# Optimization experiments

Measured on AMD Instinct MI355X. Metric: run time of the kernel, lower is better.

Reference implementation:

```python
import jax, jax.numpy as jnp
import numpy as np

N_NODES = 20000
N_EDGES = 320000
D_IN = 32 * 32 * 3  # 3072


def gcn_layer(x, W, b, src, dst):
    # Lign GCN(nn.Linear): dense transform, then sum-aggregation over edges
    h = x @ W + b                                            # [N, d_out]
    msg = jax.ops.segment_sum(h[src], dst, num_segments=N_NODES)  # neighbor sum
    return h + msg                                           # self + neighbors


def setup_inputs() -> dict:
    key = jax.random.key(0)
    ks = jax.random.split(key, 12)
    def w(k, shape, fan_in):
        return jax.random.normal(k, shape, jnp.float32) * (1.0 / np.sqrt(fan_in))
    return {
        "features": jax.random.normal(ks[0], (N_NODES, D_IN), jnp.float32),
        "src": jax.random.randint(ks[1], (N_EDGES,), 0, N_NODES),
        "dst": jax.random.randint(ks[2], (N_EDGES,), 0, N_NODES),
        "W1": w(ks[3], (D_IN, 1000), D_IN), "b1": jnp.zeros((1000,), jnp.float32),
        "W2": w(ks[4], (1000, 300), 1000), "b2": jnp.zeros((300,), jnp.float32),
        "W3": w(ks[5], (300, 20), 300),    "b3": jnp.zeros((20,), jnp.float32),
        "W4": w(ks[6], (20, 10), 20),      "b4": jnp.zeros((10,), jnp.float32),
    }


def reference(features, src, dst, W1, b1, W2, b2, W3, b3, W4, b4):
    x = features.reshape(-1, D_IN)
    x = jax.nn.relu(gcn_layer(x, W1, b1, src, dst))
    x = jax.nn.relu(gcn_layer(x, W2, b2, src, dst))
    x = gcn_layer(x, W3, b3, src, dst)
    return jnp.tanh(gcn_layer(x, W4, b4, src, dst))
```

## Files before the change

### kernel.cpp

```cpp
#include <hip/hip_runtime.h>
#include <math.h>

#define N_NODES 20000
#define N_EDGES 320000
#define D_IN    3072

#define M_PAD   20096
#define N1_PAD  1024
#define LDH1    1024
#define K2_PAD  1024
#define N2_PAD  384
#define LDH2    384

typedef short bf16x8 __attribute__((ext_vector_type(8)));
typedef float f32x4  __attribute__((ext_vector_type(4)));
typedef int   i32x4  __attribute__((ext_vector_type(4)));

#define GLOAD_LDS16(g, l) __builtin_amdgcn_global_load_lds( \
    (const __attribute__((address_space(1))) void*)(g),     \
    (__attribute__((address_space(3))) void*)(l), 16, 0, 0)

__device__ inline unsigned short f2bf(float x) {
    union { float f; unsigned u; } v; v.f = x;
    unsigned r = (v.u + 0x7FFFu + ((v.u >> 16) & 1u)) >> 16;
    return (unsigned short)r;
}
__device__ inline float bf2f(unsigned short h) {
    union { float f; unsigned u; } v; v.u = ((unsigned)h) << 16;
    return v.f;
}


__global__ void zero_counts_kernel(int* __restrict__ counts) {
    int i = blockIdx.x * blockDim.x + threadIdx.x;
    if (i < N_NODES) counts[i] = 0;
}

__global__ void count_kernel(const int* __restrict__ dst, int* __restrict__ counts) {
    int e = blockIdx.x * blockDim.x + threadIdx.x;
    if (e < N_EDGES) atomicAdd(&counts[dst[e]], 1);
}

__global__ void scan_kernel(const int* __restrict__ counts, int* __restrict__ row_start,
                            int* __restrict__ cursor) {
    __shared__ int part[1024];
    const int T = 1024;
    int t = threadIdx.x;
    const int chunk = (N_NODES + T - 1) / T;
    int lo = t * chunk;
    int hi = lo + chunk; if (hi > N_NODES) hi = N_NODES;
    int s = 0;
    for (int i = lo; i < hi; ++i) s += counts[i];
    part[t] = s;
    __syncthreads();
    for (int off = 1; off < T; off <<= 1) {
        int v = (t >= off) ? part[t - off] : 0;
        __syncthreads();
        part[t] += v;
        __syncthreads();
    }
    int run = part[t] - s;
    for (int i = lo; i < hi; ++i) {
        row_start[i] = run;
        cursor[i] = run;
        run += counts[i];
    }
    if (t == T - 1) row_start[N_NODES] = run;
}

__global__ void scatter_kernel(const int* __restrict__ src, const int* __restrict__ dst,
                               int* __restrict__ cursor, int* __restrict__ esrc) {
    int e = blockIdx.x * blockDim.x + threadIdx.x;
    if (e < N_EDGES) {
        int pos = atomicAdd(&cursor[dst[e]], 1);
        esrc[pos] = src[e];
    }
}


__global__ __launch_bounds__(256)
void convA_i8_kernel(const float* __restrict__ X, signed char* __restrict__ Aq1,
                     signed char* __restrict__ Aq2, float* __restrict__ sA) {
    __shared__ float red[256];
    const int row = blockIdx.x;
    const int t = threadIdx.x;
    const float* xr = X + (size_t)row * D_IN;
    float v[12];
    float mx = 0.f;
    #pragma unroll
    for (int c = 0; c < 3; ++c) {
        float4 f = *reinterpret_cast<const float4*>(&xr[(t + c * 256) * 4]);
        v[c*4+0] = f.x; v[c*4+1] = f.y; v[c*4+2] = f.z; v[c*4+3] = f.w;
        mx = fmaxf(mx, fmaxf(fmaxf(fabsf(f.x), fabsf(f.y)), fmaxf(fabsf(f.z), fabsf(f.w))));
    }
    red[t] = mx;
    __syncthreads();
    for (int off = 128; off > 0; off >>= 1) {
        if (t < off) red[t] = fmaxf(red[t], red[t + off]);
        __syncthreads();
    }
    const float rmax = red[0];
    const float s   = (rmax > 0.f) ? rmax / 16256.f : 1.f;
    const float inv = 16256.f / ((rmax > 0.f) ? rmax : 1.f);
    if (t == 0) sA[row] = s;
    #pragma unroll
    for (int c = 0; c < 3; ++c) {
        signed char q1v[4], q2v[4];
        #pragma unroll
        for (int e = 0; e < 4; ++e) {
            int q = __float2int_rn(v[c*4+e] * inv);
            q = min(max(q, -16256), 16256);
            int q1 = (q + 64) >> 7;
            int q2 = q - (q1 << 7);
            q1v[e] = (signed char)q1; q2v[e] = (signed char)q2;
        }
        size_t base = (size_t)row * D_IN + (size_t)(t + c * 256) * 4;
        *reinterpret_cast<char4*>(&Aq1[base]) = make_char4(q1v[0], q1v[1], q1v[2], q1v[3]);
        *reinterpret_cast<char4*>(&Aq2[base]) = make_char4(q2v[0], q2v[1], q2v[2], q2v[3]);
    }
}


__global__ __launch_bounds__(256)
void zero_swbits_kernel(unsigned* __restrict__ bits, int NPAD) {
    int n = blockIdx.x * blockDim.x + threadIdx.x;
    if (n < NPAD) bits[n] = 0u;
}

__global__ __launch_bounds__(256)
void colmaxW_kernel(const float* __restrict__ W, unsigned* __restrict__ bits,
                    int K, int N, int KCHUNK) {
    int n = blockIdx.x * blockDim.x + threadIdx.x;
    if (n >= N) return;
    int k0 = blockIdx.y * KCHUNK;
    int k1 = min(k0 + KCHUNK, K);
    float mx = 0.f;
    for (int k = k0; k < k1; ++k)
        mx = fmaxf(mx, fabsf(W[(size_t)k * N + n]));
    atomicMax(&bits[n], __float_as_uint(mx));
}

__global__ __launch_bounds__(256)
void finalize_sw_kernel(unsigned* __restrict__ bits, float* __restrict__ sW, int NPAD) {
    int n = blockIdx.x * blockDim.x + threadIdx.x;
    if (n >= NPAD) return;
    float mx = __uint_as_float(bits[n]);
    sW[n] = (mx > 0.f) ? mx / 16256.f : 1.f;
}

__global__ __launch_bounds__(256)
void convW_i8_kernel(const float* __restrict__ W, const float* __restrict__ sW,
                     signed char* __restrict__ Wq1T, signed char* __restrict__ Wq2T,
                     int K, int N, int K_PAD) {
    __shared__ float sh[32][33];
    const int t  = threadIdx.x;
    const int tx = t & 31;
    const int ty = t >> 5;
    const int n0 = blockIdx.x * 32;
    const int k0 = blockIdx.y * 32;
    #pragma unroll
    for (int it = 0; it < 4; ++it) {
        int k = k0 + ty + it * 8;
        int n = n0 + tx;
        sh[ty + it * 8][tx] = (k < K && n < N) ? W[(size_t)k * N + n] : 0.f;
    }
    __syncthreads();
    #pragma unroll
    for (int it = 0; it < 4; ++it) {
        int n = n0 + ty + it * 8;
        int k = k0 + tx;
        float v = sh[tx][ty + it * 8];
        float s = sW[n];
        int q = __float2int_rn(v / s);
        q = min(max(q, -16256), 16256);
        int q1 = (q + 64) >> 7;
        int q2 = q - (q1 << 7);
        Wq1T[(size_t)n * K_PAD + k] = (signed char)q1;
        Wq2T[(size_t)n * K_PAD + k] = (signed char)q2;
    }
}


#define GBM 128
#define GBN 128

#define ISSUE2I(p0, p1, ss) do { \
    GLOAD_LDS16(p0, &lds[ss][wid * 1024]); \
    GLOAD_LDS16(p1, &lds[ss][wid * 1024 + 4096]); \
    p0 += 64; p1 += 64; } while (0)

template <int OUTBF>
__global__ __launch_bounds__(256, 2)
void gemm_i8_mfma_kernel(const signed char* __restrict__ Aq1,
                         const signed char* __restrict__ Aq2,
                         const signed char* __restrict__ Bq1T,
                         const signed char* __restrict__ Bq2T,
                         const float* __restrict__ sA, const float* __restrict__ sB,
                         const float* __restrict__ bias, void* __restrict__ Hout,
                         int K, int NB, int ldh, int nbias) {
    __shared__ __align__(16) char lds[4][8192];

    const int t    = threadIdx.x;
    const int wid  = t >> 6;
    const int lane = t & 63;
    const int wr   = wid >> 1;
    const int wc   = wid & 1;

    const int orig = blockIdx.x;
    const int nwg  = gridDim.x;
    const int xcd  = orig & 7, loc = orig >> 3;
    const int q    = nwg >> 3, r = nwg & 7;
    const int wgid = (xcd < r ? xcd * (q + 1) : r * (q + 1) + (xcd - r) * q) + loc;
    const int m0   = (wgid / NB) * GBM;
    const int n0   = (wgid % NB) * GBN;

    i32x4 accH[4][4] = {};
    i32x4 accM[4][4] = {};

    const int byt0 = wid * 1024 + lane * 16;
    const int byt1 = byt0 + 4096;
    const int r0 = byt0 >> 6, r1 = byt1 >> 6;
    const int cs0 = (byt0 & 63) ^ (((r0 >> 1) & 3) << 4);
    const int cs1 = (byt1 & 63) ^ (((r1 >> 1) & 3) << 4);

    const signed char* pA10 = Aq1  + (size_t)(m0 + r0) * K + cs0;
    const signed char* pA11 = Aq1  + (size_t)(m0 + r1) * K + cs1;
    const signed char* pA20 = Aq2  + (size_t)(m0 + r0) * K + cs0;
    const signed char* pA21 = Aq2  + (size_t)(m0 + r1) * K + cs1;
    const signed char* pB10 = Bq1T + (size_t)(n0 + r0) * K + cs0;
    const signed char* pB11 = Bq1T + (size_t)(n0 + r1) * K + cs1;
    const signed char* pB20 = Bq2T + (size_t)(n0 + r0) * K + cs0;
    const signed char* pB21 = Bq2T + (size_t)(n0 + r1) * K + cs1;

    const int fr   = lane & 15;
    const int kbs  = ((lane >> 4) << 4) ^ (((fr >> 1) & 3) << 4);
    const int arow = wr * 64;
    const int brow = wc * 64;

    ISSUE2I(pA10, pA11, 0);
    ISSUE2I(pB10, pB11, 2);
    ISSUE2I(pB20, pB21, 3);
    ISSUE2I(pA20, pA21, 1);

    const int NT = K >> 6;
    i32x4 a1[4], b1[4], b2[4], a2[4];

    for (int tt = 0; tt < NT; ++tt) {
        if (tt == 0) asm volatile("s_waitcnt vmcnt(4)" ::: "memory");
        else         asm volatile("s_waitcnt vmcnt(2)" ::: "memory");
        __builtin_amdgcn_s_barrier();
        #pragma unroll
        for (int i = 0; i < 4; ++i)
            a1[i] = *(const i32x4*)(&lds[0][(arow + i * 16 + fr) * 64 + kbs]);
        #pragma unroll
        for (int j = 0; j < 4; ++j)
            b1[j] = *(const i32x4*)(&lds[2][(brow + j * 16 + fr) * 64 + kbs]);
        if (tt > 0) ISSUE2I(pA20, pA21, 1);
        __builtin_amdgcn_s_setprio(1);
        #pragma unroll
        for (int i = 0; i < 4; ++i)
            #pragma unroll
            for (int j = 0; j < 4; ++j)
                accH[i][j] = __builtin_amdgcn_mfma_i32_16x16x64_i8(a1[i], b1[j], accH[i][j], 0, 0, 0);
        __builtin_amdgcn_s_setprio(0);
        asm volatile("s_waitcnt vmcnt(2)" ::: "memory");
        __builtin_amdgcn_s_barrier();
        #pragma unroll
        for (int j = 0; j < 4; ++j)
            b2[j] = *(const i32x4*)(&lds[3][(brow + j * 16 + fr) * 64 + kbs]);
        if (tt < NT - 1) {
            ISSUE2I(pA10, pA11, 0);
            ISSUE2I(pB10, pB11, 2);
        }
        __builtin_amdgcn_s_setprio(1);
        #pragma unroll
        for (int i = 0; i < 4; ++i)
            #pragma unroll
            for (int j = 0; j < 4; ++j)
                accM[i][j] = __builtin_amdgcn_mfma_i32_16x16x64_i8(a1[i], b2[j], accM[i][j], 0, 0, 0);
        __builtin_amdgcn_s_setprio(0);
        if (tt < NT - 1) asm volatile("s_waitcnt vmcnt(4)" ::: "memory");
        else             asm volatile("s_waitcnt vmcnt(0)" ::: "memory");
        __builtin_amdgcn_s_barrier();
        #pragma unroll
        for (int i = 0; i < 4; ++i)
            a2[i] = *(const i32x4*)(&lds[1][(arow + i * 16 + fr) * 64 + kbs]);
        if (tt < NT - 1) ISSUE2I(pB20, pB21, 3);
        __builtin_amdgcn_s_setprio(1);
        #pragma unroll
        for (int i = 0; i < 4; ++i)
            #pragma unroll
            for (int j = 0; j < 4; ++j)
                accM[i][j] = __builtin_amdgcn_mfma_i32_16x16x64_i8(a2[i], b1[j], accM[i][j], 0, 0, 0);
        __builtin_amdgcn_s_setprio(0);
    }

    #pragma unroll
    for (int i = 0; i < 4; ++i) {
        #pragma unroll
        for (int j = 0; j < 4; ++j) {
            int row = m0 + wr * 64 + i * 16 + (lane >> 4) * 4;
            int col = n0 + wc * 64 + j * 16 + (lane & 15);
            float bv = (col < nbias) ? bias[col] : 0.f;
            float sw = sB[col];
            #pragma unroll
            for (int r2 = 0; r2 < 4; ++r2) {
                float sa = sA[row + r2];
                float v = sa * sw * (16384.f * (float)accH[i][j][r2] + 128.f * (float)accM[i][j][r2]) + bv;
                if (OUTBF) ((unsigned short*)Hout)[(size_t)(row + r2) * ldh + col] = f2bf(v);
                else       ((float*)Hout)[(size_t)(row + r2) * ldh + col] = v;
            }
        }
    }
}


#define BM 64
#define BN 64
#define BKT 16
#define TM 4
#define TN 4

__global__ __launch_bounds__(256)
void gemm_bias_kernel(const float* __restrict__ X, const float* __restrict__ W,
                      const float* __restrict__ bias, float* __restrict__ H,
                      int M, int N, int K) {
    __shared__ float As[BKT][BM];
    __shared__ float Bs[BKT][BN];

    const int t  = threadIdx.x;
    const int tx = t & 15;
    const int ty = t >> 4;
    const int m0 = blockIdx.y * BM;
    const int n0 = blockIdx.x * BN;

    float acc[TM][TN] = {};

    const int arow = t >> 2;
    const int ak0  = (t & 3) * 4;
    const int brow = t >> 4;
    const int bn0  = (t & 15) * 4;

    for (int k0 = 0; k0 < K; k0 += BKT) {
        {
            float4 v = make_float4(0.f, 0.f, 0.f, 0.f);
            int gm = m0 + arow;
            int gk = k0 + ak0;
            if (gm < M) {
                if (gk + 3 < K) {
                    v = *reinterpret_cast<const float4*>(&X[(long)gm * K + gk]);
                } else {
                    float tmp[4] = {0.f, 0.f, 0.f, 0.f};
                    for (int i = 0; i < 4; ++i)
                        if (gk + i < K) tmp[i] = X[(long)gm * K + gk + i];
                    v = make_float4(tmp[0], tmp[1], tmp[2], tmp[3]);
                }
            }
            As[ak0 + 0][arow] = v.x;
            As[ak0 + 1][arow] = v.y;
            As[ak0 + 2][arow] = v.z;
            As[ak0 + 3][arow] = v.w;
        }
        {
            float4 v = make_float4(0.f, 0.f, 0.f, 0.f);
            int gk = k0 + brow;
            int gn = n0 + bn0;
            if (gk < K) {
                if (gn + 3 < N) {
                    v = *reinterpret_cast<const float4*>(&W[(long)gk * N + gn]);
                } else {
                    float tmp[4] = {0.f, 0.f, 0.f, 0.f};
                    for (int i = 0; i < 4; ++i)
                        if (gn + i < N) tmp[i] = W[(long)gk * N + gn + i];
                    v = make_float4(tmp[0], tmp[1], tmp[2], tmp[3]);
                }
            }
            *reinterpret_cast<float4*>(&Bs[brow][bn0]) = v;
        }
        __syncthreads();

        #pragma unroll
        for (int kk = 0; kk < BKT; ++kk) {
            float a[TM], b[TN];
            *reinterpret_cast<float4*>(a) = *reinterpret_cast<const float4*>(&As[kk][ty * TM]);
            *reinterpret_cast<float4*>(b) = *reinterpret_cast<const float4*>(&Bs[kk][tx * TN]);
            #pragma unroll
            for (int i = 0; i < TM; ++i)
                #pragma unroll
                for (int j = 0; j < TN; ++j)
                    acc[i][j] += a[i] * b[j];
        }
        __syncthreads();
    }

    #pragma unroll
    for (int i = 0; i < TM; ++i) {
        int gm = m0 + ty * TM + i;
        if (gm >= M) continue;
        #pragma unroll
        for (int j = 0; j < TN; ++j) {
            int gn = n0 + tx * TN + j;
            if (gn < N) H[(long)gm * N + gn] = acc[i][j] + bias[gn];
        }
    }
}


__global__ __launch_bounds__(256)
void aggregate_i8_kernel(const unsigned short* __restrict__ H1,
                         const int* __restrict__ row_start, const int* __restrict__ esrc,
                         signed char* __restrict__ Xq1, signed char* __restrict__ Xq2,
                         float* __restrict__ sX, int d, int ld_in, int kpad) {
    __shared__ float red[256];
    const int node = blockIdx.x;
    const int t = threadIdx.x;
    const int f = t * 4;
    const int beg = row_start[node];
    const int end = row_start[node + 1];

    float a[4] = {0.f, 0.f, 0.f, 0.f};
    if (f < d) {
        ushort4 v = *reinterpret_cast<const ushort4*>(&H1[(size_t)node * ld_in + f]);
        a[0] = bf2f(v.x); a[1] = bf2f(v.y); a[2] = bf2f(v.z); a[3] = bf2f(v.w);
        for (int i = beg; i < end; ++i) {
            ushort4 w = *reinterpret_cast<const ushort4*>(&H1[(size_t)esrc[i] * ld_in + f]);
            a[0] += bf2f(w.x); a[1] += bf2f(w.y); a[2] += bf2f(w.z); a[3] += bf2f(w.w);
        }
        a[0] = fmaxf(a[0], 0.f); a[1] = fmaxf(a[1], 0.f);
        a[2] = fmaxf(a[2], 0.f); a[3] = fmaxf(a[3], 0.f);
    }
    float mx = fmaxf(fmaxf(a[0], a[1]), fmaxf(a[2], a[3]));
    red[t] = mx;
    __syncthreads();
    for (int off = 128; off > 0; off >>= 1) {
        if (t < off) red[t] = fmaxf(red[t], red[t + off]);
        __syncthreads();
    }
    const float rmax = red[0];
    const float s   = (rmax > 0.f) ? rmax / 16256.f : 1.f;
    const float inv = 16256.f / ((rmax > 0.f) ? rmax : 1.f);
    if (t == 0) sX[node] = s;
    if (f < kpad) {
        signed char q1v[4], q2v[4];
        #pragma unroll
        for (int e = 0; e < 4; ++e) {
            int q = (f < d) ? __float2int_rn(a[e] * inv) : 0;
            q = min(max(q, 0), 16256);
            int q1 = (q + 64) >> 7;
            int q2 = q - (q1 << 7);
            q1v[e] = (signed char)q1; q2v[e] = (signed char)q2;
        }
        *reinterpret_cast<char4*>(&Xq1[(size_t)node * kpad + f]) = make_char4(q1v[0], q1v[1], q1v[2], q1v[3]);
        *reinterpret_cast<char4*>(&Xq2[(size_t)node * kpad + f]) = make_char4(q2v[0], q2v[1], q2v[2], q2v[3]);
    }
}

__global__ __launch_bounds__(128)
void agg2_gemm3_kernel(const float* __restrict__ H2, const int* __restrict__ row_start,
                       const int* __restrict__ esrc, const float* __restrict__ W3,
                       const float* __restrict__ b3, float* __restrict__ h3) {
    __shared__ float x3s[304];
    __shared__ float part[6][20];
    const int node = blockIdx.x;
    const int t = threadIdx.x;
    const int beg = row_start[node];
    const int end = row_start[node + 1];
    if (t < 75) {
        const int f = t * 4;
        float4 acc = *reinterpret_cast<const float4*>(&H2[(size_t)node * LDH2 + f]);
        for (int i = beg; i < end; ++i) {
            float4 v = *reinterpret_cast<const float4*>(&H2[(size_t)esrc[i] * LDH2 + f]);
            acc.x += v.x; acc.y += v.y; acc.z += v.z; acc.w += v.w;
        }
        x3s[f + 0] = fmaxf(acc.x, 0.f);
        x3s[f + 1] = fmaxf(acc.y, 0.f);
        x3s[f + 2] = fmaxf(acc.z, 0.f);
        x3s[f + 3] = fmaxf(acc.w, 0.f);
    }
    __syncthreads();
    if (t < 120) {
        const int j = t % 20, g = t / 20;
        float s = 0.f;
        #pragma unroll 5
        for (int k = g * 50; k < g * 50 + 50; ++k)
            s += x3s[k] * W3[k * 20 + j];
        part[g][j] = s;
    }
    __syncthreads();
    if (t < 20) {
        float s = b3[t];
        #pragma unroll
        for (int g = 0; g < 6; ++g) s += part[g][t];
        h3[(size_t)node * 20 + t] = s;
    }
}

__global__ __launch_bounds__(64)
void agg3_gemm4_kernel(const float* __restrict__ h3, const int* __restrict__ row_start,
                       const int* __restrict__ esrc, const float* __restrict__ W4,
                       const float* __restrict__ b4, float* __restrict__ h4) {
    __shared__ float x4s[20];
    const int node = blockIdx.x;
    const int t = threadIdx.x;
    const int beg = row_start[node];
    const int end = row_start[node + 1];
    if (t < 20) {
        float acc = h3[(size_t)node * 20 + t];
        for (int i = beg; i < end; ++i)
            acc += h3[(size_t)esrc[i] * 20 + t];
        x4s[t] = acc;
    }
    __syncthreads();
    if (t < 10) {
        float s = b4[t];
        #pragma unroll
        for (int k = 0; k < 20; ++k) s += x4s[k] * W4[k * 10 + t];
        h4[(size_t)node * 10 + t] = s;
    }
}

template <int ACT>
__global__ __launch_bounds__(64)
void aggregate_small_kernel(const float* __restrict__ H, const int* __restrict__ row_start,
                            const int* __restrict__ esrc, float* __restrict__ out,
                            int d, int ld_in, int ld_out) {
    const int node = blockIdx.x;
    const int f = threadIdx.x;
    if (f >= d) return;
    const int beg = row_start[node];
    const int end = row_start[node + 1];
    float acc = H[(size_t)node * ld_in + f];
    for (int i = beg; i < end; ++i)
        acc += H[(size_t)esrc[i] * ld_in + f];
    if (ACT == 1) acc = fmaxf(acc, 0.f);
    if (ACT == 2) acc = tanhf(acc);
    out[(size_t)node * ld_out + f] = acc;
}

template <int ACT>
__global__ __launch_bounds__(256)
void aggregate_kernel(const float* __restrict__ H, const int* __restrict__ row_start,
                      const int* __restrict__ esrc, float* __restrict__ out,
                      int d, int ld_in) {
    const int node = blockIdx.x;
    const int t = threadIdx.x;
    const int beg = row_start[node];
    const int end = row_start[node + 1];
    float acc[4] = {0.f, 0.f, 0.f, 0.f};
    #pragma unroll
    for (int j = 0; j < 4; ++j) {
        int f = t + j * 256;
        if (f < d) acc[j] = H[(size_t)node * ld_in + f];
    }
    for (int i = beg; i < end; ++i) {
        const size_t b = (size_t)esrc[i] * ld_in;
        #pragma unroll
        for (int j = 0; j < 4; ++j) {
            int f = t + j * 256;
            if (f < d) acc[j] += H[b + f];
        }
    }
    #pragma unroll
    for (int j = 0; j < 4; ++j) {
        int f = t + j * 256;
        if (f < d) {
            float v = acc[j];
            if (ACT == 1) v = fmaxf(v, 0.f);
            if (ACT == 2) v = tanhf(v);
            out[(size_t)node * d + f] = v;
        }
    }
}


extern "C" void kernel_launch(void* const* d_in, const int* in_sizes, int n_in,
                              void* d_out, int out_size, void* d_ws, size_t ws_size,
                              hipStream_t stream) {
    const float* features = (const float*)d_in[0];
    const int*   src      = (const int*)d_in[1];
    const int*   dst      = (const int*)d_in[2];
    const float* W1 = (const float*)d_in[3];  const float* b1 = (const float*)d_in[4];
    const float* W2 = (const float*)d_in[5];  const float* b2 = (const float*)d_in[6];
    const float* W3 = (const float*)d_in[7];  const float* b3 = (const float*)d_in[8];
    const float* W4 = (const float*)d_in[9];  const float* b4 = (const float*)d_in[10];
    float* out = (float*)d_out;
    char* ws = (char*)d_ws;

    const size_t SZ_AQ    = (size_t)M_PAD * D_IN;
    const size_t OFF_AQ1  = 0;
    const size_t OFF_AQ2  = SZ_AQ;
    const size_t OFF_H1   = 2 * SZ_AQ;
    const size_t SZ_H1    = (size_t)M_PAD * LDH1 * 2;
    const size_t OFF_W1Q1 = OFF_H1 + SZ_H1;
    const size_t SZ_W1Q   = (size_t)N1_PAD * D_IN;
    const size_t OFF_W1Q2 = OFF_W1Q1 + SZ_W1Q;
    const size_t OFF_SA   = OFF_W1Q2 + SZ_W1Q;
    const size_t SZ_SA    = (size_t)M_PAD * 4;
    const size_t OFF_SW1  = OFF_SA + SZ_SA;
    const size_t OFF_W2Q1 = OFF_SW1 + 4096;
    const size_t SZ_W2Q   = (size_t)N2_PAD * K2_PAD;
    const size_t OFF_W2Q2 = OFF_W2Q1 + SZ_W2Q;
    const size_t OFF_SW2  = OFF_W2Q2 + SZ_W2Q;
    const size_t OFF_SA2  = OFF_SW2 + 4096;
    const size_t OFF_CSR  = OFF_SA2 + SZ_SA;
    const size_t SZ_CSR   = (size_t)(N_NODES * 3 + 1 + N_EDGES) * 4;
    const size_t WS_NEED  = OFF_CSR + SZ_CSR;

    const size_t OFF_X2Q1 = 0;
    const size_t SZ_X2Q   = (size_t)M_PAD * K2_PAD;
    const size_t OFF_X2Q2 = SZ_X2Q;
    const size_t OFF_H2   = 2 * SZ_X2Q;
    const size_t OFF_H3   = OFF_H1;
    const size_t OFF_H4   = OFF_H1 + 1600000;

    const bool use_mfma = (ws_size >= WS_NEED);
    size_t csr_off = use_mfma ? OFF_CSR : (size_t)2 * N_NODES * 1000 * 4;
    int* counts    = (int*)(ws + csr_off);
    int* row_start = counts + N_NODES;
    int* cursor    = row_start + N_NODES + 1;
    int* esrc      = cursor + N_NODES;

    zero_counts_kernel<<<(N_NODES + 255) / 256, 256, 0, stream>>>(counts);
    count_kernel<<<(N_EDGES + 255) / 256, 256, 0, stream>>>(dst, counts);
    scan_kernel<<<1, 1024, 0, stream>>>(counts, row_start, cursor);
    scatter_kernel<<<(N_EDGES + 255) / 256, 256, 0, stream>>>(src, dst, cursor, esrc);

    if (use_mfma) {
        signed char*    Aq1   = (signed char*)(ws + OFF_AQ1);
        signed char*    Aq2   = (signed char*)(ws + OFF_AQ2);
        unsigned short* H1    = (unsigned short*)(ws + OFF_H1);
        signed char*    W1q1T = (signed char*)(ws + OFF_W1Q1);
        signed char*    W1q2T = (signed char*)(ws + OFF_W1Q2);
        float*          sA    = (float*)(ws + OFF_SA);
        float*          sW1   = (float*)(ws + OFF_SW1);
        unsigned*       sW1b  = (unsigned*)(ws + OFF_SW1);
        signed char*    W2q1T = (signed char*)(ws + OFF_W2Q1);
        signed char*    W2q2T = (signed char*)(ws + OFF_W2Q2);
        float*          sW2   = (float*)(ws + OFF_SW2);
        unsigned*       sW2b  = (unsigned*)(ws + OFF_SW2);
        signed char*    X2q1  = (signed char*)(ws + OFF_X2Q1);
        signed char*    X2q2  = (signed char*)(ws + OFF_X2Q2);
        float*          sA2   = (float*)(ws + OFF_SA2);
        float*          H2    = (float*)(ws + OFF_H2);
        float*          h3    = (float*)(ws + OFF_H3);
        float*          h4    = (float*)(ws + OFF_H4);

        convA_i8_kernel<<<N_NODES, 256, 0, stream>>>(features, Aq1, Aq2, sA);
        zero_swbits_kernel<<<N1_PAD / 256, 256, 0, stream>>>(sW1b, N1_PAD);
        colmaxW_kernel<<<dim3((1000 + 255) / 256, 24), 256, 0, stream>>>(W1, sW1b, D_IN, 1000, 128);
        finalize_sw_kernel<<<N1_PAD / 256, 256, 0, stream>>>(sW1b, sW1, N1_PAD);
        convW_i8_kernel<<<dim3(N1_PAD / 32, D_IN / 32), 256, 0, stream>>>(
            W1, sW1, W1q1T, W1q2T, D_IN, 1000, D_IN);
        gemm_i8_mfma_kernel<1><<<(N1_PAD / GBN) * (M_PAD / GBM), 256, 0, stream>>>(
            Aq1, Aq2, W1q1T, W1q2T, sA, sW1, b1, H1, D_IN, N1_PAD / GBN, LDH1, 1000);
        aggregate_i8_kernel<<<N_NODES, 256, 0, stream>>>(
            H1, row_start, esrc, X2q1, X2q2, sA2, 1000, LDH1, K2_PAD);

        zero_swbits_kernel<<<(N2_PAD + 255) / 256, 256, 0, stream>>>(sW2b, N2_PAD);
        colmaxW_kernel<<<dim3((300 + 255) / 256, 8), 256, 0, stream>>>(W2, sW2b, 1000, 300, 128);
        finalize_sw_kernel<<<(N2_PAD + 255) / 256, 256, 0, stream>>>(sW2b, sW2, N2_PAD);
        convW_i8_kernel<<<dim3(N2_PAD / 32, K2_PAD / 32), 256, 0, stream>>>(
            W2, sW2, W2q1T, W2q2T, 1000, 300, K2_PAD);
        gemm_i8_mfma_kernel<0><<<(N2_PAD / GBN) * (M_PAD / GBM), 256, 0, stream>>>(
            X2q1, X2q2, W2q1T, W2q2T, sA2, sW2, b2, H2, K2_PAD, N2_PAD / GBN, LDH2, 300);

        agg2_gemm3_kernel<<<N_NODES, 128, 0, stream>>>(H2, row_start, esrc, W3, b3, h3);
        agg3_gemm4_kernel<<<N_NODES, 64, 0, stream>>>(h3, row_start, esrc, W4, b4, h4);
        aggregate_small_kernel<2><<<N_NODES, 64, 0, stream>>>(h4, row_start, esrc, out, 10, 10, 10);
    } else {
        const size_t BUF = (size_t)N_NODES * 1000 * 4;
        float* bufA = (float*)ws;
        float* bufB = (float*)(ws + BUF);

        dim3 g1((1000 + BN - 1) / BN, (N_NODES + BM - 1) / BM);
        gemm_bias_kernel<<<g1, 256, 0, stream>>>(features, W1, b1, bufA, N_NODES, 1000, D_IN);
        aggregate_kernel<1><<<N_NODES, 256, 0, stream>>>(bufA, row_start, esrc, bufB, 1000, 1000);

        dim3 g2((300 + BN - 1) / BN, (N_NODES + BM - 1) / BM);
        gemm_bias_kernel<<<g2, 256, 0, stream>>>(bufB, W2, b2, bufA, N_NODES, 300, 1000);
        aggregate_kernel<1><<<N_NODES, 256, 0, stream>>>(bufA, row_start, esrc, bufB, 300, 300);

        dim3 g3((20 + BN - 1) / BN, (N_NODES + BM - 1) / BM);
        gemm_bias_kernel<<<g3, 256, 0, stream>>>(bufB, W3, b3, bufA, N_NODES, 20, 300);
        aggregate_kernel<0><<<N_NODES, 256, 0, stream>>>(bufA, row_start, esrc, bufB, 20, 20);

        dim3 g4((10 + BN - 1) / BN, (N_NODES + BM - 1) / BM);
        gemm_bias_kernel<<<g4, 256, 0, stream>>>(bufB, W4, b4, bufA, N_NODES, 10, 20);
        aggregate_kernel<2><<<N_NODES, 256, 0, stream>>>(bufA, row_start, esrc, out, 10, 10);
    }
}
```

Measured before the change: 665.6 us.

## Fuse weight scale and quantization kernels and store layer-2 output as bf16

```diff
diff --git a/kernel.cpp b/kernel.cpp
--- a/kernel.cpp
+++ b/kernel.cpp
@@ -122,61 +122,52 @@
 
 
 __global__ __launch_bounds__(256)
-void zero_swbits_kernel(unsigned* __restrict__ bits, int NPAD) {
-    int n = blockIdx.x * blockDim.x + threadIdx.x;
-    if (n < NPAD) bits[n] = 0u;
-}
-
-__global__ __launch_bounds__(256)
-void colmaxW_kernel(const float* __restrict__ W, unsigned* __restrict__ bits,
-                    int K, int N, int KCHUNK) {
-    int n = blockIdx.x * blockDim.x + threadIdx.x;
-    if (n >= N) return;
-    int k0 = blockIdx.y * KCHUNK;
-    int k1 = min(k0 + KCHUNK, K);
-    float mx = 0.f;
-    for (int k = k0; k < k1; ++k)
-        mx = fmaxf(mx, fabsf(W[(size_t)k * N + n]));
-    atomicMax(&bits[n], __float_as_uint(mx));
-}
-
-__global__ __launch_bounds__(256)
-void finalize_sw_kernel(unsigned* __restrict__ bits, float* __restrict__ sW, int NPAD) {
-    int n = blockIdx.x * blockDim.x + threadIdx.x;
-    if (n >= NPAD) return;
-    float mx = __uint_as_float(bits[n]);
-    sW[n] = (mx > 0.f) ? mx / 16256.f : 1.f;
-}
-
-__global__ __launch_bounds__(256)
-void convW_i8_kernel(const float* __restrict__ W, const float* __restrict__ sW,
-                     signed char* __restrict__ Wq1T, signed char* __restrict__ Wq2T,
-                     int K, int N, int K_PAD) {
+void quantW_i8_kernel(const float* __restrict__ W, signed char* __restrict__ Wq1T,
+                      signed char* __restrict__ Wq2T, float* __restrict__ sW,
+                      int K, int N, int K_PAD) {
+    __shared__ float red[8][32];
     __shared__ float sh[32][33];
+    __shared__ float sinv[32];
     const int t  = threadIdx.x;
     const int tx = t & 31;
-    const int ty = t >> 5;
+    const int kr = t >> 5;
     const int n0 = blockIdx.x * 32;
-    const int k0 = blockIdx.y * 32;
-    #pragma unroll
-    for (int it = 0; it < 4; ++it) {
-        int k = k0 + ty + it * 8;
-        int n = n0 + tx;
-        sh[ty + it * 8][tx] = (k < K && n < N) ? W[(size_t)k * N + n] : 0.f;
-    }
-    __syncthreads();
-    #pragma unroll
-    for (int it = 0; it < 4; ++it) {
-        int n = n0 + ty + it * 8;
-        int k = k0 + tx;
-        float v = sh[tx][ty + it * 8];
-        float s = sW[n];
-        int q = __float2int_rn(v / s);
-        q = min(max(q, -16256), 16256);
-        int q1 = (q + 64) >> 7;
-        int q2 = q - (q1 << 7);
-        Wq1T[(size_t)n * K_PAD + k] = (signed char)q1;
-        Wq2T[(size_t)n * K_PAD + k] = (signed char)q2;
+    const int n  = n0 + tx;
+    float mx = 0.f;
+    if (n < N)
+        for (int k = kr; k < K; k += 8)
+            mx = fmaxf(mx, fabsf(W[(size_t)k * N + n]));
+    red[kr][tx] = mx;
+    __syncthreads();
+    if (kr == 0) {
+        float m = red[0][tx];
+        #pragma unroll
+        for (int r = 1; r < 8; ++r) m = fmaxf(m, red[r][tx]);
+        sW[n] = (m > 0.f) ? m / 16256.f : 1.f;
+        sinv[tx] = 16256.f / ((m > 0.f) ? m : 1.f);
+    }
+    __syncthreads();
+    for (int k0 = 0; k0 < K_PAD; k0 += 32) {
+        #pragma unroll
+        for (int it = 0; it < 4; ++it) {
+            int k = k0 + kr + it * 8;
+            sh[kr + it * 8][tx] = (k < K && n < N) ? W[(size_t)k * N + n] : 0.f;
+        }
+        __syncthreads();
+        #pragma unroll
+        for (int it = 0; it < 4; ++it) {
+            int nn = n0 + kr + it * 8;
+            int k  = k0 + tx;
+            float v = sh[tx][kr + it * 8];
+            float inv = sinv[kr + it * 8];
+            int q = __float2int_rn(v * inv);
+            q = min(max(q, -16256), 16256);
+            int q1 = (q + 64) >> 7;
+            int q2 = q - (q1 << 7);
+            Wq1T[(size_t)nn * K_PAD + k] = (signed char)q1;
+            Wq2T[(size_t)nn * K_PAD + k] = (signed char)q2;
+        }
+        __syncthreads();
     }
 }
 
@@ -456,7 +447,7 @@
 }
 
 __global__ __launch_bounds__(128)
-void agg2_gemm3_kernel(const float* __restrict__ H2, const int* __restrict__ row_start,
+void agg2_gemm3_kernel(const unsigned short* __restrict__ H2, const int* __restrict__ row_start,
                        const int* __restrict__ esrc, const float* __restrict__ W3,
                        const float* __restrict__ b3, float* __restrict__ h3) {
     __shared__ float x3s[304];
@@ -467,15 +458,16 @@
     const int end = row_start[node + 1];
     if (t < 75) {
         const int f = t * 4;
-        float4 acc = *reinterpret_cast<const float4*>(&H2[(size_t)node * LDH2 + f]);
+        ushort4 v = *reinterpret_cast<const ushort4*>(&H2[(size_t)node * LDH2 + f]);
+        float a0 = bf2f(v.x), a1 = bf2f(v.y), a2 = bf2f(v.z), a3 = bf2f(v.w);
         for (int i = beg; i < end; ++i) {
-            float4 v = *reinterpret_cast<const float4*>(&H2[(size_t)esrc[i] * LDH2 + f]);
-            acc.x += v.x; acc.y += v.y; acc.z += v.z; acc.w += v.w;
-        }
-        x3s[f + 0] = fmaxf(acc.x, 0.f);
-        x3s[f + 1] = fmaxf(acc.y, 0.f);
-        x3s[f + 2] = fmaxf(acc.z, 0.f);
-        x3s[f + 3] = fmaxf(acc.w, 0.f);
+            ushort4 w = *reinterpret_cast<const ushort4*>(&H2[(size_t)esrc[i] * LDH2 + f]);
+            a0 += bf2f(w.x); a1 += bf2f(w.y); a2 += bf2f(w.z); a3 += bf2f(w.w);
+        }
+        x3s[f + 0] = fmaxf(a0, 0.f);
+        x3s[f + 1] = fmaxf(a1, 0.f);
+        x3s[f + 2] = fmaxf(a2, 0.f);
+        x3s[f + 3] = fmaxf(a3, 0.f);
     }
     __syncthreads();
     if (t < 120) {
@@ -633,35 +625,25 @@
         signed char*    W1q2T = (signed char*)(ws + OFF_W1Q2);
         float*          sA    = (float*)(ws + OFF_SA);
         float*          sW1   = (float*)(ws + OFF_SW1);
-        unsigned*       sW1b  = (unsigned*)(ws + OFF_SW1);
         signed char*    W2q1T = (signed char*)(ws + OFF_W2Q1);
         signed char*    W2q2T = (signed char*)(ws + OFF_W2Q2);
         float*          sW2   = (float*)(ws + OFF_SW2);
-        unsigned*       sW2b  = (unsigned*)(ws + OFF_SW2);
         signed char*    X2q1  = (signed char*)(ws + OFF_X2Q1);
         signed char*    X2q2  = (signed char*)(ws + OFF_X2Q2);
         float*          sA2   = (float*)(ws + OFF_SA2);
-        float*          H2    = (float*)(ws + OFF_H2);
+        unsigned short* H2    = (unsigned short*)(ws + OFF_H2);
         float*          h3    = (float*)(ws + OFF_H3);
         float*          h4    = (float*)(ws + OFF_H4);
 
         convA_i8_kernel<<<N_NODES, 256, 0, stream>>>(features, Aq1, Aq2, sA);
-        zero_swbits_kernel<<<N1_PAD / 256, 256, 0, stream>>>(sW1b, N1_PAD);
-        colmaxW_kernel<<<dim3((1000 + 255) / 256, 24), 256, 0, stream>>>(W1, sW1b, D_IN, 1000, 128);
-        finalize_sw_kernel<<<N1_PAD / 256, 256, 0, stream>>>(sW1b, sW1, N1_PAD);
-        convW_i8_kernel<<<dim3(N1_PAD / 32, D_IN / 32), 256, 0, stream>>>(
-            W1, sW1, W1q1T, W1q2T, D_IN, 1000, D_IN);
+        quantW_i8_kernel<<<N1_PAD / 32, 256, 0, stream>>>(W1, W1q1T, W1q2T, sW1, D_IN, 1000, D_IN);
         gemm_i8_mfma_kernel<1><<<(N1_PAD / GBN) * (M_PAD / GBM), 256, 0, stream>>>(
             Aq1, Aq2, W1q1T, W1q2T, sA, sW1, b1, H1, D_IN, N1_PAD / GBN, LDH1, 1000);
         aggregate_i8_kernel<<<N_NODES, 256, 0, stream>>>(
             H1, row_start, esrc, X2q1, X2q2, sA2, 1000, LDH1, K2_PAD);
 
-        zero_swbits_kernel<<<(N2_PAD + 255) / 256, 256, 0, stream>>>(sW2b, N2_PAD);
-        colmaxW_kernel<<<dim3((300 + 255) / 256, 8), 256, 0, stream>>>(W2, sW2b, 1000, 300, 128);
-        finalize_sw_kernel<<<(N2_PAD + 255) / 256, 256, 0, stream>>>(sW2b, sW2, N2_PAD);
-        convW_i8_kernel<<<dim3(N2_PAD / 32, K2_PAD / 32), 256, 0, stream>>>(
-            W2, sW2, W2q1T, W2q2T, 1000, 300, K2_PAD);
-        gemm_i8_mfma_kernel<0><<<(N2_PAD / GBN) * (M_PAD / GBM), 256, 0, stream>>>(
+        quantW_i8_kernel<<<N2_PAD / 32, 256, 0, stream>>>(W2, W2q1T, W2q2T, sW2, 1000, 300, K2_PAD);
+        gemm_i8_mfma_kernel<1><<<(N2_PAD / GBN) * (M_PAD / GBM), 256, 0, stream>>>(
             X2q1, X2q2, W2q1T, W2q2T, sA2, sW2, b2, H2, K2_PAD, N2_PAD / GBN, LDH2, 300);
 
         agg2_gemm3_kernel<<<N_NODES, 128, 0, stream>>>(H2, row_start, esrc, W3, b3, h3);
```

Result: slower. 814.3 us (+22.4%).
